# Performance work log

Hardware: AMD Instinct MI355X
Metric: run time of the kernel (lower is better)

The kernel has to match this reference:

```python
import jax, jax.numpy as jnp
import numpy as np

ROW, IN_DIM, OUT_DIM, BATCH = 64, 1024, 1024, 512


def setup_inputs() -> dict:
    key = jax.random.key(0)
    k1, k2, k3 = jax.random.split(key, 3)
    x = jax.random.normal(k1, (BATCH, ROW, IN_DIM), dtype=jnp.float32)
    # torch.nn.Linear init: U(-1/sqrt(in_dim), 1/sqrt(in_dim)) for weight and bias
    bound = 1.0 / np.sqrt(IN_DIM)
    W = jax.random.uniform(k2, (ROW, IN_DIM, OUT_DIM), minval=-bound, maxval=bound, dtype=jnp.float32)
    b = jax.random.uniform(k3, (ROW, OUT_DIM), minval=-bound, maxval=bound, dtype=jnp.float32)
    return {"x": x, "W": W, "b": b}


def reference(x, W, b):
    # per-row Linear fused into a single grouped GEMM:
    # out[b, r, o] = sum_i x[b, r, i] * W[r, i, o] + b[r, o]
    return jnp.einsum('bri,rio->bro', x, W) + b[None, :, :]
```

## Files before the change

### kernel.cpp

```cpp
#include <hip/hip_runtime.h>
#include <hip/hip_bf16.h>

#define NROW  64
#define KDIM  1024
#define NDIM  1024

typedef short bf16x8 __attribute__((ext_vector_type(8)));
typedef float f32x4  __attribute__((ext_vector_type(4)));

__device__ __forceinline__ unsigned pk2bf(float lo, float hi) {
  unsigned ulo = __builtin_bit_cast(unsigned, lo) + 0x8000u;
  unsigned uhi = __builtin_bit_cast(unsigned, hi) + 0x8000u;
  return __builtin_amdgcn_perm(uhi, ulo, 0x07060302u);
}

__global__ __launch_bounds__(512, 2) void Group_MLP_kernel(
    const float* __restrict__ x, const float* __restrict__ W,
    const float* __restrict__ bias, float* __restrict__ out) {
  const int g   = blockIdx.x;
  const int xcd = g & 7;
  const int idx = g >> 3;
  const int r   = xcd * 8 + (idx >> 3);
  const int mb  = (idx >> 2) & 1;
  const int nb  = idx & 3;
  const int m0 = mb * 256;
  const int n0 = nb * 256;

  const int t    = threadIdx.x;
  const int l    = t & 63;
  const int wave = t >> 6;
  const int wm   = wave >> 2, wn = wave & 3;
  const int lm   = l & 15, quad = l >> 4;

  __shared__ uint4 smem4[2048];
  uint2* s2 = (uint2*)smem4;

  const int maBase = ((t >> 7) << 4) | ((t >> 1) & 15);
  const int kof    = (((t >> 5) & 3) << 3) | ((t & 1) << 2);
  const float* gA[4];
  #pragma unroll
  for (int i = 0; i < 4; ++i)
    gA[i] = x + (size_t)(m0 + i * 64 + maBase) * (NROW * KDIM) + r * KDIM + kof;

  const int n4 = ((t >> 3) & 1) | (((t >> 5) & 1) << 1) | (((t >> 1) & 1) << 2)
               | (((t >> 2) & 1) << 3) | (((t >> 4) & 1) << 4) | (((t >> 6) & 1) << 5);
  const int qh = (t & 1) | (((t >> 7) & 1) << 1) | (((t >> 8) & 1) << 2);
  const float* gB[4];
  #pragma unroll
  for (int j = 0; j < 4; ++j)
    gB[j] = W + (size_t)r * (KDIM * NDIM) + (qh * 4 + j) * NDIM + n0 + n4 * 4;
  const int baseP  = (n4 >> 2) * 64 + ((qh >> 1) & 3) * 16 + (n4 & 3) * 4;
  const int swBase = baseP ^ ((n4 >> 2) & 7);
  const int hB     = qh & 1;
  const int bW     = 2048 | (swBase << 1) | hB;

  int aIdx[8], bIdx[4];
  #pragma unroll
  for (int i = 0; i < 8; ++i) aIdx[i] = (wm * 8 + i) * 64 + l;
  #pragma unroll
  for (int j = 0; j < 4; ++j) {
    int grp = wn * 4 + j;
    bIdx[j] = 1024 + grp * 64 + (l ^ (grp & 7));
  }

  f32x4 acc[8][4];
  #pragma unroll
  for (int i = 0; i < 8; ++i)
    #pragma unroll
    for (int j = 0; j < 4; ++j)
      acc[i][j] = {0.f, 0.f, 0.f, 0.f};

  float4 rawA[4], rawB[4];
  uint2  cvtA[4], cvtB[4];

  #pragma unroll
  for (int i = 0; i < 4; ++i) rawA[i] = *(const float4*)(gA[i]);
  #pragma unroll
  for (int j = 0; j < 4; ++j) rawB[j] = *(const float4*)(gB[j]);

  #pragma unroll
  for (int i = 0; i < 4; ++i) {
    cvtA[i].x = pk2bf(rawA[i].x, rawA[i].y);
    cvtA[i].y = pk2bf(rawA[i].z, rawA[i].w);
  }
  cvtB[0].x = pk2bf(rawB[0].x, rawB[1].x); cvtB[0].y = pk2bf(rawB[2].x, rawB[3].x);
  cvtB[1].x = pk2bf(rawB[0].y, rawB[1].y); cvtB[1].y = pk2bf(rawB[2].y, rawB[3].y);
  cvtB[2].x = pk2bf(rawB[0].z, rawB[1].z); cvtB[2].y = pk2bf(rawB[2].z, rawB[3].z);
  cvtB[3].x = pk2bf(rawB[0].w, rawB[1].w); cvtB[3].y = pk2bf(rawB[2].w, rawB[3].w);

  #pragma unroll
  for (int i = 0; i < 4; ++i) { gA[i] += 32; rawA[i] = *(const float4*)(gA[i]); }
  #pragma unroll
  for (int j = 0; j < 4; ++j) { gB[j] += 32 * NDIM; rawB[j] = *(const float4*)(gB[j]); }

  for (int ks = 0; ks < 32; ++ks) {
    __syncthreads();
    #pragma unroll
    for (int i = 0; i < 4; ++i) s2[i * 512 + t] = cvtA[i];
    #pragma unroll
    for (int cc = 0; cc < 4; ++cc) s2[bW ^ (cc << 1)] = cvtB[cc];
    __syncthreads();

    bf16x8 af[8], bfr[4];
    #pragma unroll
    for (int i = 0; i < 8; ++i) af[i]  = __builtin_bit_cast(bf16x8, smem4[aIdx[i]]);
    #pragma unroll
    for (int j = 0; j < 4; ++j) bfr[j] = __builtin_bit_cast(bf16x8, smem4[bIdx[j]]);

    if (ks < 31) {
      #pragma unroll
      for (int i = 0; i < 4; ++i) {
        cvtA[i].x = pk2bf(rawA[i].x, rawA[i].y);
        cvtA[i].y = pk2bf(rawA[i].z, rawA[i].w);
      }
      cvtB[0].x = pk2bf(rawB[0].x, rawB[1].x); cvtB[0].y = pk2bf(rawB[2].x, rawB[3].x);
      cvtB[1].x = pk2bf(rawB[0].y, rawB[1].y); cvtB[1].y = pk2bf(rawB[2].y, rawB[3].y);
      cvtB[2].x = pk2bf(rawB[0].z, rawB[1].z); cvtB[2].y = pk2bf(rawB[2].z, rawB[3].z);
      cvtB[3].x = pk2bf(rawB[0].w, rawB[1].w); cvtB[3].y = pk2bf(rawB[2].w, rawB[3].w);
      if (ks < 30) {
        #pragma unroll
        for (int i = 0; i < 4; ++i) { gA[i] += 32; rawA[i] = *(const float4*)(gA[i]); }
        #pragma unroll
        for (int j = 0; j < 4; ++j) { gB[j] += 32 * NDIM; rawB[j] = *(const float4*)(gB[j]); }
      }
    }

    #pragma unroll
    for (int j = 0; j < 4; ++j)
      #pragma unroll
      for (int i = 0; i < 8; ++i)
        acc[i][j] = __builtin_amdgcn_mfma_f32_16x16x32_bf16(af[i], bfr[j], acc[i][j], 0, 0, 0);
  }

  const int nColBase = n0 + wn * 64 + lm;
  const int mRowBase = m0 + wm * 128 + quad * 4;
  #pragma unroll
  for (int j = 0; j < 4; ++j) {
    int n = nColBase + j * 16;
    float bv = bias[r * NDIM + n];
    #pragma unroll
    for (int i = 0; i < 8; ++i) {
      int mr = mRowBase + i * 16;
      #pragma unroll
      for (int v = 0; v < 4; ++v) {
        out[(size_t)(mr + v) * (NROW * NDIM) + r * NDIM + n] = acc[i][j][v] + bv;
      }
    }
  }
}

extern "C" void kernel_launch(void* const* d_in, const int* in_sizes, int n_in,
                              void* d_out, int out_size, void* d_ws, size_t ws_size,
                              hipStream_t stream) {
  const float* x    = (const float*)d_in[0];
  const float* W    = (const float*)d_in[1];
  const float* bias = (const float*)d_in[2];
  float* out        = (float*)d_out;
  dim3 grid(512), block(512);
  hipLaunchKernelGGL(Group_MLP_kernel, grid, block, 0, stream, x, W, bias, out);
}
```

Measured before the change: 513.1 us.

## Double-buffer LDS tiles with one barrier per k-step and raise MFMA priority

Shared memory is doubled so the next k-tile is converted and stored into the alternate buffer while MFMAs consume the current one. This removes one of the two barriers per k-step and lets global loads, conversion and LDS writes overlap with the matrix math. MFMA blocks are wrapped in s_setprio to favour the math waves. The launch bound's minimum-occupancy hint is raised from 2 to 4. That may cap registers per thread below what the 128-float accumulator plus fragments need, which risks spills.

```diff
diff --git a/kernel.cpp b/kernel.cpp
--- a/kernel.cpp
+++ b/kernel.cpp
@@ -14,7 +14,7 @@
   return __builtin_amdgcn_perm(uhi, ulo, 0x07060302u);
 }
 
-__global__ __launch_bounds__(512, 2) void Group_MLP_kernel(
+__global__ __launch_bounds__(512, 4) void Group_MLP_kernel(
     const float* __restrict__ x, const float* __restrict__ W,
     const float* __restrict__ bias, float* __restrict__ out) {
   const int g   = blockIdx.x;
@@ -32,7 +32,7 @@
   const int wm   = wave >> 2, wn = wave & 3;
   const int lm   = l & 15, quad = l >> 4;
 
-  __shared__ uint4 smem4[2048];
+  __shared__ uint4 smem4[4096];
   uint2* s2 = (uint2*)smem4;
 
   const int maBase = ((t >> 7) << 4) | ((t >> 1) & 15);
@@ -73,64 +73,74 @@
   float4 rawA[4], rawB[4];
   uint2  cvtA[4], cvtB[4];
 
+#define CONVERT_ALL()                                                              \
+  {                                                                                \
+    _Pragma("unroll")                                                              \
+    for (int i = 0; i < 4; ++i) {                                                  \
+      cvtA[i].x = pk2bf(rawA[i].x, rawA[i].y);                                     \
+      cvtA[i].y = pk2bf(rawA[i].z, rawA[i].w);                                     \
+    }                                                                              \
+    cvtB[0].x = pk2bf(rawB[0].x, rawB[1].x); cvtB[0].y = pk2bf(rawB[2].x, rawB[3].x); \
+    cvtB[1].x = pk2bf(rawB[0].y, rawB[1].y); cvtB[1].y = pk2bf(rawB[2].y, rawB[3].y); \
+    cvtB[2].x = pk2bf(rawB[0].z, rawB[1].z); cvtB[2].y = pk2bf(rawB[2].z, rawB[3].z); \
+    cvtB[3].x = pk2bf(rawB[0].w, rawB[1].w); cvtB[3].y = pk2bf(rawB[2].w, rawB[3].w); \
+  }
+
+#define ADVANCE_LOAD()                                                             \
+  {                                                                                \
+    _Pragma("unroll")                                                              \
+    for (int i = 0; i < 4; ++i) { gA[i] += 32; rawA[i] = *(const float4*)(gA[i]); } \
+    _Pragma("unroll")                                                              \
+    for (int j = 0; j < 4; ++j) { gB[j] += 32 * NDIM; rawB[j] = *(const float4*)(gB[j]); } \
+  }
+
   #pragma unroll
   for (int i = 0; i < 4; ++i) rawA[i] = *(const float4*)(gA[i]);
   #pragma unroll
   for (int j = 0; j < 4; ++j) rawB[j] = *(const float4*)(gB[j]);
+  CONVERT_ALL();
+  #pragma unroll
+  for (int i = 0; i < 4; ++i) s2[i * 512 + t] = cvtA[i];
+  #pragma unroll
+  for (int cc = 0; cc < 4; ++cc) s2[bW ^ (cc << 1)] = cvtB[cc];
+  ADVANCE_LOAD();
+  __syncthreads();
 
-  #pragma unroll
-  for (int i = 0; i < 4; ++i) {
-    cvtA[i].x = pk2bf(rawA[i].x, rawA[i].y);
-    cvtA[i].y = pk2bf(rawA[i].z, rawA[i].w);
+#define STEP(KS, CUR, NXT)                                                         \
+  {                                                                                \
+    bf16x8 af[8], bfr[4];                                                          \
+    _Pragma("unroll")                                                              \
+    for (int i = 0; i < 8; ++i)                                                    \
+      af[i]  = __builtin_bit_cast(bf16x8, smem4[aIdx[i] + (CUR) * 2048]);          \
+    _Pragma("unroll")                                                              \
+    for (int j = 0; j < 4; ++j)                                                    \
+      bfr[j] = __builtin_bit_cast(bf16x8, smem4[bIdx[j] + (CUR) * 2048]);          \
+    if ((KS) < 31) {                                                               \
+      CONVERT_ALL();                                                               \
+      _Pragma("unroll")                                                            \
+      for (int i = 0; i < 4; ++i) s2[i * 512 + t + (NXT) * 4096] = cvtA[i];        \
+      _Pragma("unroll")                                                            \
+      for (int cc = 0; cc < 4; ++cc) s2[(bW ^ (cc << 1)) + (NXT) * 4096] = cvtB[cc]; \
+      if ((KS) < 30) ADVANCE_LOAD();                                               \
+    }                                                                              \
+    __builtin_amdgcn_s_setprio(1);                                                 \
+    _Pragma("unroll")                                                              \
+    for (int j = 0; j < 4; ++j)                                                    \
+      _Pragma("unroll")                                                            \
+      for (int i = 0; i < 8; ++i)                                                  \
+        acc[i][j] = __builtin_amdgcn_mfma_f32_16x16x32_bf16(af[i], bfr[j], acc[i][j], 0, 0, 0); \
+    __builtin_amdgcn_s_setprio(0);                                                 \
+    __syncthreads();                                                               \
   }
-  cvtB[0].x = pk2bf(rawB[0].x, rawB[1].x); cvtB[0].y = pk2bf(rawB[2].x, rawB[3].x);
-  cvtB[1].x = pk2bf(rawB[0].y, rawB[1].y); cvtB[1].y = pk2bf(rawB[2].y, rawB[3].y);
-  cvtB[2].x = pk2bf(rawB[0].z, rawB[1].z); cvtB[2].y = pk2bf(rawB[2].z, rawB[3].z);
-  cvtB[3].x = pk2bf(rawB[0].w, rawB[1].w); cvtB[3].y = pk2bf(rawB[2].w, rawB[3].w);
 
-  #pragma unroll
-  for (int i = 0; i < 4; ++i) { gA[i] += 32; rawA[i] = *(const float4*)(gA[i]); }
-  #pragma unroll
-  for (int j = 0; j < 4; ++j) { gB[j] += 32 * NDIM; rawB[j] = *(const float4*)(gB[j]); }
+  for (int kp = 0; kp < 16; ++kp) {
+    STEP(2 * kp,     0, 1);
+    STEP(2 * kp + 1, 1, 0);
+  }
 
-  for (int ks = 0; ks < 32; ++ks) {
-    __syncthreads();
-    #pragma unroll
-    for (int i = 0; i < 4; ++i) s2[i * 512 + t] = cvtA[i];
-    #pragma unroll
-    for (int cc = 0; cc < 4; ++cc) s2[bW ^ (cc << 1)] = cvtB[cc];
-    __syncthreads();
-
-    bf16x8 af[8], bfr[4];
-    #pragma unroll
-    for (int i = 0; i < 8; ++i) af[i]  = __builtin_bit_cast(bf16x8, smem4[aIdx[i]]);
-    #pragma unroll
-    for (int j = 0; j < 4; ++j) bfr[j] = __builtin_bit_cast(bf16x8, smem4[bIdx[j]]);
-
-    if (ks < 31) {
-      #pragma unroll
-      for (int i = 0; i < 4; ++i) {
-        cvtA[i].x = pk2bf(rawA[i].x, rawA[i].y);
-        cvtA[i].y = pk2bf(rawA[i].z, rawA[i].w);
-      }
-      cvtB[0].x = pk2bf(rawB[0].x, rawB[1].x); cvtB[0].y = pk2bf(rawB[2].x, rawB[3].x);
-      cvtB[1].x = pk2bf(rawB[0].y, rawB[1].y); cvtB[1].y = pk2bf(rawB[2].y, rawB[3].y);
-      cvtB[2].x = pk2bf(rawB[0].z, rawB[1].z); cvtB[2].y = pk2bf(rawB[2].z, rawB[3].z);
-      cvtB[3].x = pk2bf(rawB[0].w, rawB[1].w); cvtB[3].y = pk2bf(rawB[2].w, rawB[3].w);
-      if (ks < 30) {
-        #pragma unroll
-        for (int i = 0; i < 4; ++i) { gA[i] += 32; rawA[i] = *(const float4*)(gA[i]); }
-        #pragma unroll
-        for (int j = 0; j < 4; ++j) { gB[j] += 32 * NDIM; rawB[j] = *(const float4*)(gB[j]); }
-      }
-    }
-
-    #pragma unroll
-    for (int j = 0; j < 4; ++j)
-      #pragma unroll
-      for (int i = 0; i < 8; ++i)
-        acc[i][j] = __builtin_amdgcn_mfma_f32_16x16x32_bf16(af[i], bfr[j], acc[i][j], 0, 0, 0);
-  }
+#undef STEP
+#undef ADVANCE_LOAD
+#undef CONVERT_ALL
 
   const int nColBase = n0 + wn * 64 + lm;
   const int mRowBase = m0 + wm * 128 + quad * 4;
```

Result: slower. 1.642 ms (+220.1%).
